# Optimization experiments

Hardware: AMD Instinct MI355X
Metric: run time of the kernel (lower is better)

The kernel has to match this reference:

```python
import jax, jax.numpy as jnp
import numpy as np

N, C, H, W = 32, 256, 56, 56   # batch, channels (inplanes == planes), spatial
EPS = 1e-5                     # BatchNorm eps (PyTorch default)
THR = 0.5                      # mask_hard_threshold (hard_inference mode)


def conv3x3(x, w):
    # stride 1, padding 1, no bias -- matches conv3x3() in the source
    return jax.lax.conv_general_dilated(
        x, w, window_strides=(1, 1), padding=((1, 1), (1, 1)),
        dimension_numbers=('NCHW', 'OIHW', 'NCHW'))


def bn_inf(y, g, b, mu, v):
    # inference-mode BatchNorm: per-channel affine with running stats
    s = (g * jax.lax.rsqrt(v + EPS))[None, :, None, None]
    return y * s + (b - mu * g * jax.lax.rsqrt(v + EPS))[None, :, None, None]


def setup_inputs() -> dict:
    key = jax.random.key(0)
    ks = jax.random.split(key, 10)
    x = jax.random.normal(ks[0], (N, C, H, W), jnp.float32)
    # main conv weights (3x3, no bias)
    w1 = jax.random.normal(ks[1], (C, C, 3, 3), jnp.float32) * 0.05
    w2 = jax.random.normal(ks[2], (C, C, 3, 3), jnp.float32) * 0.05
    # BN params (running stats)
    g1 = jnp.ones((C,), jnp.float32); b1 = jnp.zeros((C,), jnp.float32)
    mu1 = jax.random.normal(ks[3], (C,), jnp.float32) * 0.1
    v1 = jax.random.uniform(ks[4], (C,), jnp.float32, 0.5, 1.5)
    g2 = jnp.ones((C,), jnp.float32); b2 = jnp.zeros((C,), jnp.float32)
    mu2 = jax.random.normal(ks[5], (C,), jnp.float32) * 0.1
    v2 = jax.random.uniform(ks[6], (C,), jnp.float32, 0.5, 1.5)
    # mask convs: Conv2d(C, 1, 3, stride=1, pad=1) with bias; random weights so the
    wm1 = jax.random.normal(ks[7], (1, C, 3, 3), jnp.float32) * 0.05
    bm1 = jnp.zeros((1,), jnp.float32)
    wm2 = jax.random.normal(ks[8], (1, C, 3, 3), jnp.float32) * 0.05
    bm2 = jnp.zeros((1,), jnp.float32)
    return dict(x=x, w1=w1, w2=w2, g1=g1, b1=b1, mu1=mu1, v1=v1,
                g2=g2, b2=b2, mu2=mu2, v2=v2,
                wm1=wm1, bm1=bm1, wm2=wm2, bm2=bm2)


def reference(x, w1, w2, g1, b1, mu1, v1, g2, b2, mu2, v2, wm1, bm1, wm2, bm2):
    # Gumbel-Sigmoid gates in hard_inference mode: sigmoid(mask_conv(x)) > threshold.
    # [N,1,H,W] hard masks (non-differentiable constants w.r.t. the gate).
    m1 = (jax.nn.sigmoid(conv3x3(x, wm1) + bm1[None, :, None, None]) > THR).astype(x.dtype)
    m2 = (jax.nn.sigmoid(conv3x3(x, wm2) + bm2[None, :, None, None]) > THR).astype(x.dtype)
    # apply_proxy_dcn_bn_relu: gather patches at mask_loc -> matmul(W) -> BN -> ReLU
    # -> scatter (zeros elsewhere). Dense-equivalent: relu(bn(conv(x))) * mask.
    out = jax.nn.relu(bn_inf(conv3x3(x, w1), g1, b1, mu1, v1)) * m1
    # second conv: gather -> matmul -> BN -> scatter (ReLU applied after residual)
    out = bn_inf(conv3x3(out, w2), g2, b2, mu2, v2) * m2
    # residual add (identity: stride=1, inplanes==planes -> no downsample) + ReLU
    return jax.nn.relu(out + x)
```

## Files before the change

### kernel.cpp

```cpp
#include <hip/hip_runtime.h>
#include <hip/hip_bf16.h>


#define NB 32
#define C  256
#define H  56
#define W  56
#define HW (H*W)
#define NBHW (NB*HW)
#define EPSV 1e-5f
#define WELEM (C*C*9)
#define MSPL 2
#define MCH (C/MSPL)

typedef __hip_bfloat16 bf16;
typedef __attribute__((ext_vector_type(8))) short  bf16x8;
typedef __attribute__((ext_vector_type(4))) float  floatx4;

__device__ __forceinline__ void async_copy16(void* lds, const void* gptr) {
    __builtin_amdgcn_global_load_lds(
        (const __attribute__((address_space(1))) unsigned int*)gptr,
        (__attribute__((address_space(3))) unsigned int*)lds, 16, 0, 0);
}

__global__ __launch_bounds__(128) void wcvt_kernel(
    const float* __restrict__ wm1, const float* __restrict__ wm2,
    double* __restrict__ wd)
{
    int i = blockIdx.x * 128 + threadIdx.x;
    if (i >= C * 18) return;
    int c = i / 18;
    int r = i - c * 18;
    int m = r / 9;
    int t = r - 9 * m;
    const float* src = m ? wm2 : wm1;
    wd[i] = (double)src[c * 9 + t];
}

__global__ __launch_bounds__(128) void mask_part_kernel(
    const float* __restrict__ x, const double* __restrict__ wd,
    double* __restrict__ z)
{
    int pixb  = blockIdx.x >> 1;
    int split = blockIdx.x & 1;
    int idx = pixb * 128 + threadIdx.x;
    int n  = idx / HW;
    int hw = idx - n * HW;

    const float*  xp = x  + (size_t)n * C * HW + (size_t)split * MCH * HW + hw;
    const double* wp = wd + (size_t)split * MCH * 18;

    double acc[18];
    #pragma unroll
    for (int j = 0; j < 18; ++j) acc[j] = 0.0;

    for (int c = 0; c < MCH; ++c) {
        double xv = (double)xp[(size_t)c * HW];
        const double* w = wp + c * 18;
        #pragma unroll
        for (int j = 0; j < 18; ++j)
            acc[j] += xv * w[j];
    }

    #pragma unroll
    for (int j = 0; j < 18; ++j)
        z[(size_t)(split * 18 + j) * NBHW + idx] = acc[j];
}

__global__ __launch_bounds__(256) void mask_reduce_kernel(
    const double* __restrict__ z,
    const float* __restrict__ bm1, const float* __restrict__ bm2,
    float* __restrict__ m1, float* __restrict__ m2)
{
    int idx = blockIdx.x * 256 + threadIdx.x;
    int n  = idx / HW;
    int hw = idx - n * HW;
    int h  = hw / W;
    int w_ = hw - h * W;

    double a1 = (double)bm1[0], a2 = (double)bm2[0];
    #pragma unroll
    for (int ky = 0; ky < 3; ++ky) {
        int y = h + ky - 1;
        if ((unsigned)y >= (unsigned)H) continue;
        #pragma unroll
        for (int kx = 0; kx < 3; ++kx) {
            int xx = w_ + kx - 1;
            if ((unsigned)xx >= (unsigned)W) continue;
            int t = ky * 3 + kx;
            size_t q = (size_t)n * HW + (size_t)y * W + xx;
            a1 += z[(size_t)(0 * 18 + 0 * 9 + t) * NBHW + q]
                + z[(size_t)(1 * 18 + 0 * 9 + t) * NBHW + q];
            a2 += z[(size_t)(0 * 18 + 1 * 9 + t) * NBHW + q]
                + z[(size_t)(1 * 18 + 1 * 9 + t) * NBHW + q];
        }
    }
    m1[idx] = (a1 > 0.0) ? 1.0f : 0.0f;
    m2[idx] = (a2 > 0.0) ? 1.0f : 0.0f;
}

__global__ __launch_bounds__(256) void transpose_kernel(
    const float* __restrict__ x, bf16* __restrict__ xb)
{
    __shared__ float tile[64][65];
    int bid = blockIdx.x;
    int pt = bid % 49; bid /= 49;
    int ct = bid % 4;  int n = bid / 4;
    int p0 = pt * 64, c0 = ct * 64;
    int tl = threadIdx.x & 63;
    int tg = threadIdx.x >> 6;
    const float* xp = x + ((size_t)(n*C + c0) * HW) + p0;
    #pragma unroll
    for (int i = 0; i < 16; ++i) {
        int cl = tg*16 + i;
        tile[cl][tl] = xp[(size_t)cl * HW + tl];
    }
    __syncthreads();
    bf16* op = xb + ((size_t)(n*HW + p0) * C) + c0;
    #pragma unroll
    for (int i = 0; i < 16; ++i) {
        int pl = tg*16 + i;
        op[(size_t)pl * C + tl] = __float2bfloat16(tile[tl][pl]);
    }
}

__global__ __launch_bounds__(256) void pack_kernel(
    const float* __restrict__ w1, const float* __restrict__ w2,
    bf16* __restrict__ w1p, bf16* __restrict__ w2p)
{
    int idx = blockIdx.x * 256 + threadIdx.x;
    const float* src = (idx < WELEM) ? w1 : w2;
    bf16* dst        = (idx < WELEM) ? w1p : w2p;
    int f = (idx < WELEM) ? idx : idx - WELEM;
    int e  = f & 7;
    int O  = f >> 3;
    int L  = O & 63;
    int j  = (O >> 6) & 15;
    int ks = (O >> 10) & 7;
    int t  = O >> 13;
    int co = j*16 + (L & 15);
    int ci = ks*32 + ((L >> 4) & 3)*8 + e;
    dst[f] = __float2bfloat16(src[((size_t)co*C + ci)*9 + t]);
}

template<bool FIRST>
__global__ __launch_bounds__(256, 2) void conv_mfma(
    const bf16* __restrict__ inb,
    const bf16* __restrict__ wp,
    const float* __restrict__ g,  const float* __restrict__ b,
    const float* __restrict__ mu, const float* __restrict__ vv,
    const float* __restrict__ mask,
    const float* __restrict__ xres,
    bf16* __restrict__ outb,
    float* __restrict__ outf)
{
    __shared__ uint4 albufq[800];
    __shared__ uint4 bbufq[2][1024];
    __shared__ float msk[128];
    short* albuf = (short*)albufq;

    int tid = threadIdx.x;
    int L   = tid & 63;
    int wv  = tid >> 6;

    int bid = (int)blockIdx.x;
    bid = (bid & 7) * 98 + (bid >> 3);

    int t0g = bid * 2;
    int n0 = t0g / 49, tl0 = t0g - n0 * 49;
    int y0a = (tl0 / 7) * 8, x0a = (tl0 % 7) * 8;
    size_t ibasea = (size_t)n0 * HW * C;
    int t1g = t0g + 1;
    int n1 = t1g / 49, tl1 = t1g - n1 * 49;
    int y0b = (tl1 / 7) * 8, x0b = (tl1 % 7) * 8;
    size_t ibaseb = (size_t)n1 * HW * C;

    if (tid < 128) {
        int s  = tid >> 6;
        int p  = tid & 63;
        int pr = p >> 3, pc = p & 7;
        int nn = s ? n1  : n0;
        int yy = s ? y0b : y0a;
        int xx = s ? x0b : x0a;
        msk[tid] = mask[(size_t)nn*HW + (yy+pr)*W + (xx+pc)];
    }

    int m  = L & 15;
    int kb = L >> 4;
    int a_addr[8];
    #pragma unroll
    for (int mi = 0; mi < 8; ++mi) {
        int p    = mi*16 + m;
        int sub  = p >> 6;
        int pl   = p & 63;
        int pos2 = sub*100 + (pl >> 3)*10 + (pl & 7);
        a_addr[mi] = (kb*200 + pos2) * 8;
    }
    int b_addr[4];
    #pragma unroll
    for (int jj = 0; jj < 4; ++jj)
        b_addr[jj] = ((wv*4 + jj)*64 + L) * 8;

    floatx4 acc[8][4];
    #pragma unroll
    for (int mi = 0; mi < 8; ++mi)
        #pragma unroll
        for (int jj = 0; jj < 4; ++jj)
            acc[mi][jj] = (floatx4){0.f, 0.f, 0.f, 0.f};

    auto stageA = [&](int ck) {
        for (int S = tid; S < 800; S += 256) {
            int kbg  = S / 200;
            int pos2 = S - kbg*200;
            int sub  = pos2 >= 100;
            int pos  = sub ? pos2 - 100 : pos2;
            int r  = pos / 10;
            int c  = pos - r*10;
            int yy = (sub ? y0b : y0a) + r - 1;
            int xx = (sub ? x0b : x0a) + c - 1;
            uint4 val = make_uint4(0u, 0u, 0u, 0u);
            if ((unsigned)yy < (unsigned)H && (unsigned)xx < (unsigned)W) {
                size_t ib = sub ? ibaseb : ibasea;
                val = *(const uint4*)(inb + ib + (size_t)(yy*W + xx)*C + ck*32 + kbg*8);
            }
            albufq[S] = val;
        }
    };
    auto issueB = [&](int tap, int ck, int buf) {
        const bf16* src = wp + (size_t)(tap*8 + ck) * 8192;
        short* dstb = (short*)bbufq[buf];
        #pragma unroll
        for (int i = 0; i < 4; ++i) {
            int off = (wv*4 + i) * 512;
            async_copy16(dstb + off, src + off + L*8);
        }
    };

    stageA(0);
    issueB(0, 0, 0);
    __syncthreads();

    int cur = 0;
    for (int ck = 0; ck < 8; ++ck) {
        #pragma unroll
        for (int tap = 0; tap < 9; ++tap) {
            if (tap < 8)          issueB(tap + 1, ck,     cur ^ 1);
            else if (ck < 7)      issueB(0,       ck + 1, cur ^ 1);

            const int ky = tap / 3;
            const int aoff = (ky*10 + (tap - ky*3)) * 8;
            short* bb = (short*)bbufq[cur];
            bf16x8 af[8], bfr[4];
            #pragma unroll
            for (int mi = 0; mi < 8; ++mi)
                af[mi] = *(const bf16x8*)(albuf + a_addr[mi] + aoff);
            #pragma unroll
            for (int jj = 0; jj < 4; ++jj)
                bfr[jj] = *(const bf16x8*)(bb + b_addr[jj]);
            #pragma unroll
            for (int mi = 0; mi < 8; ++mi)
                #pragma unroll
                for (int jj = 0; jj < 4; ++jj)
                    acc[mi][jj] = __builtin_amdgcn_mfma_f32_16x16x32_bf16(
                        af[mi], bfr[jj], acc[mi][jj], 0, 0, 0);

            __syncthreads();
            cur ^= 1;
        }
        if (ck < 7) {
            stageA(ck + 1);
            __syncthreads();
        }
    }

    int quad = L >> 4;
    int wbase = wv * 64;
    #pragma unroll
    for (int jj = 0; jj < 4; ++jj) {
        int co = wbase + jj*16 + (L & 15);
        float s_ = g[co] * rsqrtf(vv[co] + EPSV);
        float t_ = b[co] - mu[co] * s_;
        #pragma unroll
        for (int mi = 0; mi < 8; ++mi) {
            int pbase = mi*16 + quad*4;
            int sub   = pbase >> 6;
            int pl    = pbase & 63;
            int yy = sub ? y0b : y0a;
            int xx = sub ? x0b : x0a;
            size_t ib = sub ? ibaseb : ibasea;
            int nn = sub ? n1 : n0;
            if (FIRST) {
                #pragma unroll
                for (int r = 0; r < 4; ++r) {
                    int p = pl + r;
                    float v = acc[mi][jj][r] * s_ + t_;
                    v = fmaxf(v, 0.f) * msk[pbase + r];
                    int pg = (yy + (p >> 3))*W + (xx + (p & 7));
                    outb[ib + (size_t)pg*C + co] = __float2bfloat16(v);
                }
            } else {
                int pg = (yy + (pl >> 3))*W + (xx + (pl & 7));
                size_t oidx = ((size_t)(nn*C + co))*HW + pg;
                floatx4 xr = *(const floatx4*)(xres + oidx);
                floatx4 ov;
                #pragma unroll
                for (int r = 0; r < 4; ++r) {
                    float v = acc[mi][jj][r] * s_ + t_;
                    v = v * msk[pbase + r] + xr[r];
                    ov[r] = fmaxf(v, 0.f);
                }
                *(floatx4*)(outf + oidx) = ov;
            }
        }
    }
}

extern "C" void kernel_launch(void* const* d_in, const int* in_sizes, int n_in,
                              void* d_out, int out_size, void* d_ws, size_t ws_size,
                              hipStream_t stream) {
    const float* x   = (const float*)d_in[0];
    const float* w1  = (const float*)d_in[1];
    const float* w2  = (const float*)d_in[2];
    const float* g1  = (const float*)d_in[3];
    const float* b1  = (const float*)d_in[4];
    const float* mu1 = (const float*)d_in[5];
    const float* v1  = (const float*)d_in[6];
    const float* g2  = (const float*)d_in[7];
    const float* b2  = (const float*)d_in[8];
    const float* mu2 = (const float*)d_in[9];
    const float* v2  = (const float*)d_in[10];
    const float* wm1 = (const float*)d_in[11];
    const float* bm1 = (const float*)d_in[12];
    const float* wm2 = (const float*)d_in[13];
    const float* bm2 = (const float*)d_in[14];
    float* out = (float*)d_out;

    float* m1   = (float*)d_ws;
    float* m2   = m1 + (size_t)NBHW;
    bf16*  w1p  = (bf16*)(m2 + (size_t)NBHW);
    bf16*  w2p  = w1p + WELEM;
    bf16*  tmpb = w2p + WELEM;
    double* z   = (double*)(tmpb + (size_t)NBHW*C);
    double* wd  = z + (size_t)MSPL*18*NBHW;
    bf16*  xb   = (bf16*)d_out;

    wcvt_kernel<<<(C*18 + 127)/128, 128, 0, stream>>>(wm1, wm2, wd);
    mask_part_kernel<<<(NBHW/128)*MSPL, 128, 0, stream>>>(x, wd, z);
    mask_reduce_kernel<<<NBHW/256, 256, 0, stream>>>(z, bm1, bm2, m1, m2);
    transpose_kernel<<<NB*4*49, 256, 0, stream>>>(x, xb);
    pack_kernel<<<2*WELEM/256, 256, 0, stream>>>(w1, w2, w1p, w2p);

    const int grid = NBHW / 128;
    conv_mfma<true ><<<grid, 256, 0, stream>>>(
        xb,   w1p, g1, b1, mu1, v1, m1, nullptr, tmpb, nullptr);
    conv_mfma<false><<<grid, 256, 0, stream>>>(
        tmpb, w2p, g2, b2, mu2, v2, m2, x, nullptr, out);
}
```

Measured before the change: 603.1 us.

## Triple-buffer per-wave weight tiles and drop per-tap block barriers

Weight tiles move from a double buffer to a triple buffer, and loads are issued two taps ahead. Each wave now loads and reads only its own slice of the weights, so the per-tap __syncthreads is replaced by an explicit s_waitcnt vmcnt(8). MFMA sections are wrapped in s_setprio so compute waves get scheduling priority. This is meant to remove barrier stalls and hide global-to-LDS latency better, at the cost of a larger LDS footprint. There is a correctness risk: on the last taps of the final chunk no new loads are issued, so vmcnt(8) may not actually wait for the tile being read.

Measured after the change: 543.3 us. -9.9%, faster.

```diff
diff --git a/kernel.cpp b/kernel.cpp
--- a/kernel.cpp
+++ b/kernel.cpp
@@ -155,9 +155,10 @@
     float* __restrict__ outf)
 {
     __shared__ uint4 albufq[800];
-    __shared__ uint4 bbufq[2][1024];
+    __shared__ uint4 bbufq[3*1024];
     __shared__ float msk[128];
     short* albuf = (short*)albufq;
+    short* bbuf  = (short*)bbufq;
 
     int tid = threadIdx.x;
     int L   = tid & 63;
@@ -196,10 +197,7 @@
         int pos2 = sub*100 + (pl >> 3)*10 + (pl & 7);
         a_addr[mi] = (kb*200 + pos2) * 8;
     }
-    int b_addr[4];
-    #pragma unroll
-    for (int jj = 0; jj < 4; ++jj)
-        b_addr[jj] = ((wv*4 + jj)*64 + L) * 8;
+    int b_base = wv*2048 + L*8;
 
     floatx4 acc[8][4];
     #pragma unroll
@@ -226,48 +224,52 @@
             albufq[S] = val;
         }
     };
-    auto issueB = [&](int tap, int ck, int buf) {
-        const bf16* src = wp + (size_t)(tap*8 + ck) * 8192;
-        short* dstb = (short*)bbufq[buf];
-        #pragma unroll
-        for (int i = 0; i < 4; ++i) {
-            int off = (wv*4 + i) * 512;
-            async_copy16(dstb + off, src + off + L*8);
-        }
+    auto issueB = [&](int tap2, int ck2, int slot) {
+        const bf16* src = wp + (size_t)(tap2*8 + ck2) * 8192 + (size_t)wv*4*512 + L*8;
+        short* dstb = bbuf + (slot*4 + wv)*2048;
+        #pragma unroll
+        for (int i = 0; i < 4; ++i)
+            async_copy16(dstb + i*512, src + i*512);
     };
 
     stageA(0);
     issueB(0, 0, 0);
+    issueB(1, 0, 1);
     __syncthreads();
 
-    int cur = 0;
     for (int ck = 0; ck < 8; ++ck) {
         #pragma unroll
         for (int tap = 0; tap < 9; ++tap) {
-            if (tap < 8)          issueB(tap + 1, ck,     cur ^ 1);
-            else if (ck < 7)      issueB(0,       ck + 1, cur ^ 1);
+            if (tap < 7) {
+                issueB(tap + 2, ck, (tap + 2) % 3);
+            } else {
+                if (ck < 7) issueB(tap - 7, ck + 1, (tap - 7) % 3);
+            }
+            __builtin_amdgcn_sched_barrier(0);
+            asm volatile("s_waitcnt vmcnt(8)" ::: "memory");
+            __builtin_amdgcn_sched_barrier(0);
 
             const int ky = tap / 3;
             const int aoff = (ky*10 + (tap - ky*3)) * 8;
-            short* bb = (short*)bbufq[cur];
+            const int bslot = (tap % 3) * 4 * 2048;
             bf16x8 af[8], bfr[4];
             #pragma unroll
             for (int mi = 0; mi < 8; ++mi)
                 af[mi] = *(const bf16x8*)(albuf + a_addr[mi] + aoff);
             #pragma unroll
             for (int jj = 0; jj < 4; ++jj)
-                bfr[jj] = *(const bf16x8*)(bb + b_addr[jj]);
+                bfr[jj] = *(const bf16x8*)(bbuf + bslot + b_base + jj*512);
+            __builtin_amdgcn_s_setprio(1);
             #pragma unroll
             for (int mi = 0; mi < 8; ++mi)
                 #pragma unroll
                 for (int jj = 0; jj < 4; ++jj)
                     acc[mi][jj] = __builtin_amdgcn_mfma_f32_16x16x32_bf16(
                         af[mi], bfr[jj], acc[mi][jj], 0, 0, 0);
-
+            __builtin_amdgcn_s_setprio(0);
+        }
+        if (ck < 7) {
             __syncthreads();
-            cur ^= 1;
-        }
-        if (ck < 7) {
             stageA(ck + 1);
             __syncthreads();
         }
```
